# Performance work log

Measured on AMD Instinct MI355X. Metric: run time of the kernel, lower is better.

## Reference

```python
import jax, jax.numpy as jnp
import numpy as np

B, C, H, W_SP = 32, 384, 64, 64
R = 8  # reduced_channels for in_channels=384, ratio=16
STD = 0.02  # 'normal' init scheme


def setup_inputs() -> dict:
    key = jax.random.key(0)
    ks = jax.random.split(key, 6)
    return {
        "x": jax.random.normal(ks[0], (B, C, H, W_SP), dtype=jnp.float32),
        "W1": jax.random.normal(ks[1], (R, C), dtype=jnp.float32) * STD,      # conv1 1x1
        "W2_1": jax.random.normal(ks[2], (R, C // R), dtype=jnp.float32) * STD,  # grouped 1x1, groups=R
        "W2_2": jax.random.normal(ks[3], (R,), dtype=jnp.float32) * STD,      # grouped 1x1 on R chans (per-channel scale)
        "W3": jax.random.normal(ks[4], (R, C), dtype=jnp.float32) * STD,      # conv3 1x1
        "Wfc": jax.random.normal(ks[5], (C, 3 * R), dtype=jnp.float32) * STD, # fc 1x1
    }


def reference(x, W1, W2_1, W2_2, W3, Wfc):
    b, c, h, w = x.shape
    r = W1.shape[0]
    # fused global pools over spatial dims -> [B, C]
    avg = jnp.mean(x, axis=(2, 3))
    mx = jnp.max(x, axis=(2, 3))
    mn = jnp.min(x, axis=(2, 3))  # AdaptiveMinPool2d (unfold trick == global min)
    # 1x1 convs on 1x1-spatial tensors == matmuls
    avg_out = avg @ W1.T                                   # [B, R]
    max_out = jnp.einsum('brg,rg->br', mx.reshape(b, r, c // r), W2_1) * W2_2  # grouped convs
    min_out = mn @ W3.T                                    # [B, R]
    combined = jnp.concatenate([avg_out, max_out, min_out], axis=1)  # [B, 3R]
    logits = combined @ Wfc.T                              # [B, C]
    # broadcast residual add over spatial dims, then sigmoid
    return jax.nn.sigmoid(logits[:, :, None, None] + x)
```

## Files before the change

### kernel.cpp

```cpp
#include <hip/hip_runtime.h>
#include <hip/hip_bf16.h>

#define BATCH 32
#define CHAN 384
#define SPATIAL 4096
#define BC (BATCH * CHAN)
#define RCH 8
#define NCOMB (3 * RCH)

typedef float f32x4 __attribute__((ext_vector_type(4)));

__global__ __launch_bounds__(256) void pool_kernel(const float* __restrict__ x,
                                                   float* __restrict__ ws) {
    const int plane = blockIdx.x * 4 + (threadIdx.x >> 6);
    const int lane = threadIdx.x & 63;
    const f32x4* p4 = (const f32x4*)(x + (size_t)plane * SPATIAL);

    f32x4 vs = {0.0f, 0.0f, 0.0f, 0.0f};
    f32x4 vmx = {-__builtin_inff(), -__builtin_inff(), -__builtin_inff(), -__builtin_inff()};
    f32x4 vmn = {__builtin_inff(), __builtin_inff(), __builtin_inff(), __builtin_inff()};
#pragma unroll
    for (int k = 0; k < 16; ++k) {
        f32x4 v = p4[lane + k * 64];
        vs += v;
        vmx.x = fmaxf(vmx.x, v.x); vmx.y = fmaxf(vmx.y, v.y);
        vmx.z = fmaxf(vmx.z, v.z); vmx.w = fmaxf(vmx.w, v.w);
        vmn.x = fminf(vmn.x, v.x); vmn.y = fminf(vmn.y, v.y);
        vmn.z = fminf(vmn.z, v.z); vmn.w = fminf(vmn.w, v.w);
    }
    float s = (vs.x + vs.y) + (vs.z + vs.w);
    float mx = fmaxf(fmaxf(vmx.x, vmx.y), fmaxf(vmx.z, vmx.w));
    float mn = fminf(fminf(vmn.x, vmn.y), fminf(vmn.z, vmn.w));
#pragma unroll
    for (int off = 32; off > 0; off >>= 1) {
        s += __shfl_xor(s, off);
        mx = fmaxf(mx, __shfl_xor(mx, off));
        mn = fminf(mn, __shfl_xor(mn, off));
    }
    if (lane == 0) {
        ws[plane] = s;
        ws[BC + plane] = mx;
        ws[2 * BC + plane] = mn;
    }
}

__global__ __launch_bounds__(CHAN) void logits_kernel(
    const float* __restrict__ pools,
    const float* __restrict__ W1,
    const float* __restrict__ W2_1,
    const float* __restrict__ W2_2,
    const float* __restrict__ W3,
    const float* __restrict__ Wfc,
    float* __restrict__ logits)
{
    const int b = blockIdx.x;
    const int tid = threadIdx.x;
    __shared__ float avg[CHAN], smx[CHAN], smn[CHAN], comb[NCOMB];

    avg[tid] = pools[b * CHAN + tid] * (1.0f / (float)SPATIAL);
    smx[tid] = pools[BC + b * CHAN + tid];
    smn[tid] = pools[2 * BC + b * CHAN + tid];
    __syncthreads();

    const int gid = tid >> 4;
    const int l16 = tid & 15;
    float a = 0.0f;
    if (gid < RCH) {
        const int r = gid;
#pragma unroll
        for (int k = 0; k < CHAN / 16; ++k) {
            const int c = l16 + k * 16;
            a += avg[c] * W1[r * CHAN + c];
        }
    } else if (gid < 2 * RCH) {
        const int r = gid - RCH;
#pragma unroll
        for (int k = 0; k < 3; ++k) {
            const int g = l16 + k * 16;
            a += smx[r * (CHAN / RCH) + g] * W2_1[r * (CHAN / RCH) + g];
        }
    } else {
        const int r = gid - 2 * RCH;
#pragma unroll
        for (int k = 0; k < CHAN / 16; ++k) {
            const int c = l16 + k * 16;
            a += smn[c] * W3[r * CHAN + c];
        }
    }
#pragma unroll
    for (int off = 8; off > 0; off >>= 1) a += __shfl_xor(a, off);
    if (l16 == 0) {
        if (gid >= RCH && gid < 2 * RCH) a *= W2_2[gid - RCH];
        comb[gid] = a;
    }
    __syncthreads();

    float l = 0.0f;
#pragma unroll
    for (int j = 0; j < NCOMB; ++j) l += comb[j] * Wfc[tid * NCOMB + j];
    logits[b * CHAN + tid] = l;
}

__global__ __launch_bounds__(256) void add_sig_kernel(
    const float* __restrict__ x,
    const float* __restrict__ logits,
    float* __restrict__ out)
{
    const size_t n4 = (size_t)BC * (SPATIAL / 4);
    const size_t stride = 2048 * 256;
    size_t i = blockIdx.x * (size_t)blockDim.x + threadIdx.x;
    const f32x4* x4 = (const f32x4*)x;
    f32x4* o4 = (f32x4*)out;
    for (; i < n4; i += 2 * stride) {
        const size_t i2 = i + stride;
        f32x4 v0 = x4[i];
        f32x4 v1 = x4[i2];
        const float l0 = logits[(int)(i >> 10)];
        const float l1 = logits[(int)(i2 >> 10)];
        f32x4 o0, o1;
        o0.x = __builtin_amdgcn_rcpf(1.0f + __expf(-(v0.x + l0)));
        o0.y = __builtin_amdgcn_rcpf(1.0f + __expf(-(v0.y + l0)));
        o0.z = __builtin_amdgcn_rcpf(1.0f + __expf(-(v0.z + l0)));
        o0.w = __builtin_amdgcn_rcpf(1.0f + __expf(-(v0.w + l0)));
        o1.x = __builtin_amdgcn_rcpf(1.0f + __expf(-(v1.x + l1)));
        o1.y = __builtin_amdgcn_rcpf(1.0f + __expf(-(v1.y + l1)));
        o1.z = __builtin_amdgcn_rcpf(1.0f + __expf(-(v1.z + l1)));
        o1.w = __builtin_amdgcn_rcpf(1.0f + __expf(-(v1.w + l1)));
        __builtin_nontemporal_store(o0, &o4[i]);
        __builtin_nontemporal_store(o1, &o4[i2]);
    }
}

extern "C" void kernel_launch(void* const* d_in, const int* in_sizes, int n_in,
                              void* d_out, int out_size, void* d_ws, size_t ws_size,
                              hipStream_t stream) {
    const float* x    = (const float*)d_in[0];
    const float* W1   = (const float*)d_in[1];
    const float* W2_1 = (const float*)d_in[2];
    const float* W2_2 = (const float*)d_in[3];
    const float* W3   = (const float*)d_in[4];
    const float* Wfc  = (const float*)d_in[5];
    float* out = (float*)d_out;
    float* ws  = (float*)d_ws;
    float* logits = ws + 3 * BC;

    hipLaunchKernelGGL(pool_kernel, dim3(BC / 4), dim3(256), 0, stream, x, ws);
    hipLaunchKernelGGL(logits_kernel, dim3(BATCH), dim3(CHAN), 0, stream,
                       ws, W1, W2_1, W2_2, W3, Wfc, logits);
    hipLaunchKernelGGL(add_sig_kernel, dim3(2048), dim3(256), 0, stream,
                       x, logits, out);
}
```

Before: 95.34 us.

## Stage x copy into output during pooling and apply sigmoid in place

The pooling kernel now loads x with nontemporal hints and writes a copy of each plane into the output buffer while computing sum, max and min. The add-sigmoid kernel then reads from and writes back to the output buffer in place, using regular stores instead of nontemporal ones. The intent seems to be that the second pass reads data likely still resident in the large last-level cache, rather than re-fetching x from HBM. The cost is an extra full-tensor write in the first kernel, and the benefit depends on a roughly 200MB tensor staying in cache.

```diff
diff --git a/kernel.cpp b/kernel.cpp
--- a/kernel.cpp
+++ b/kernel.cpp
@@ -10,18 +10,21 @@
 
 typedef float f32x4 __attribute__((ext_vector_type(4)));
 
-__global__ __launch_bounds__(256) void pool_kernel(const float* __restrict__ x,
-                                                   float* __restrict__ ws) {
+__global__ __launch_bounds__(256) void pool_copy_kernel(const float* __restrict__ x,
+                                                        float* __restrict__ out,
+                                                        float* __restrict__ ws) {
     const int plane = blockIdx.x * 4 + (threadIdx.x >> 6);
     const int lane = threadIdx.x & 63;
     const f32x4* p4 = (const f32x4*)(x + (size_t)plane * SPATIAL);
+    f32x4* o4 = (f32x4*)(out + (size_t)plane * SPATIAL);
 
     f32x4 vs = {0.0f, 0.0f, 0.0f, 0.0f};
     f32x4 vmx = {-__builtin_inff(), -__builtin_inff(), -__builtin_inff(), -__builtin_inff()};
     f32x4 vmn = {__builtin_inff(), __builtin_inff(), __builtin_inff(), __builtin_inff()};
 #pragma unroll
     for (int k = 0; k < 16; ++k) {
-        f32x4 v = p4[lane + k * 64];
+        f32x4 v = __builtin_nontemporal_load(&p4[lane + k * 64]);
+        o4[lane + k * 64] = v;
         vs += v;
         vmx.x = fmaxf(vmx.x, v.x); vmx.y = fmaxf(vmx.y, v.y);
         vmx.z = fmaxf(vmx.z, v.z); vmx.w = fmaxf(vmx.w, v.w);
@@ -102,32 +105,30 @@
 }
 
 __global__ __launch_bounds__(256) void add_sig_kernel(
-    const float* __restrict__ x,
-    const float* __restrict__ logits,
-    float* __restrict__ out)
+    float* __restrict__ out,
+    const float* __restrict__ logits)
 {
     const size_t n4 = (size_t)BC * (SPATIAL / 4);
     const size_t stride = 2048 * 256;
     size_t i = blockIdx.x * (size_t)blockDim.x + threadIdx.x;
-    const f32x4* x4 = (const f32x4*)x;
     f32x4* o4 = (f32x4*)out;
     for (; i < n4; i += 2 * stride) {
         const size_t i2 = i + stride;
-        f32x4 v0 = x4[i];
-        f32x4 v1 = x4[i2];
+        f32x4 v0 = o4[i];
+        f32x4 v1 = o4[i2];
         const float l0 = logits[(int)(i >> 10)];
         const float l1 = logits[(int)(i2 >> 10)];
-        f32x4 o0, o1;
-        o0.x = __builtin_amdgcn_rcpf(1.0f + __expf(-(v0.x + l0)));
-        o0.y = __builtin_amdgcn_rcpf(1.0f + __expf(-(v0.y + l0)));
-        o0.z = __builtin_amdgcn_rcpf(1.0f + __expf(-(v0.z + l0)));
-        o0.w = __builtin_amdgcn_rcpf(1.0f + __expf(-(v0.w + l0)));
-        o1.x = __builtin_amdgcn_rcpf(1.0f + __expf(-(v1.x + l1)));
-        o1.y = __builtin_amdgcn_rcpf(1.0f + __expf(-(v1.y + l1)));
-        o1.z = __builtin_amdgcn_rcpf(1.0f + __expf(-(v1.z + l1)));
-        o1.w = __builtin_amdgcn_rcpf(1.0f + __expf(-(v1.w + l1)));
-        __builtin_nontemporal_store(o0, &o4[i]);
-        __builtin_nontemporal_store(o1, &o4[i2]);
+        f32x4 r0, r1;
+        r0.x = __builtin_amdgcn_rcpf(1.0f + __expf(-(v0.x + l0)));
+        r0.y = __builtin_amdgcn_rcpf(1.0f + __expf(-(v0.y + l0)));
+        r0.z = __builtin_amdgcn_rcpf(1.0f + __expf(-(v0.z + l0)));
+        r0.w = __builtin_amdgcn_rcpf(1.0f + __expf(-(v0.w + l0)));
+        r1.x = __builtin_amdgcn_rcpf(1.0f + __expf(-(v1.x + l1)));
+        r1.y = __builtin_amdgcn_rcpf(1.0f + __expf(-(v1.y + l1)));
+        r1.z = __builtin_amdgcn_rcpf(1.0f + __expf(-(v1.z + l1)));
+        r1.w = __builtin_amdgcn_rcpf(1.0f + __expf(-(v1.w + l1)));
+        o4[i] = r0;
+        o4[i2] = r1;
     }
 }
 
@@ -144,9 +145,10 @@
     float* ws  = (float*)d_ws;
     float* logits = ws + 3 * BC;
 
-    hipLaunchKernelGGL(pool_kernel, dim3(BC / 4), dim3(256), 0, stream, x, ws);
+    hipLaunchKernelGGL(pool_copy_kernel, dim3(BC / 4), dim3(256), 0, stream,
+                       x, out, ws);
     hipLaunchKernelGGL(logits_kernel, dim3(BATCH), dim3(CHAN), 0, stream,
                        ws, W1, W2_1, W2_2, W3, Wfc, logits);
     hipLaunchKernelGGL(add_sig_kernel, dim3(2048), dim3(256), 0, stream,
-                       x, logits, out);
+                       out, logits);
 }
```

Result: slower. 130.6 us (+36.9%).
